# Kernel optimization log

Hardware: AMD Instinct MI355X
Metric: run time of the kernel (lower is better)

## Reference

```python
import jax, jax.numpy as jnp
import numpy as np

G, NPG = 2048, 512          # glimpses, points per glimpse
N0 = G * NPG                # 1,048,576 input points
CPG, CPG2 = 128, 32         # clusters per glimpse at level1/level2
M1, M2 = G * CPG, G * CPG2  # 262144, 65536


def _seg_mean_np(x, ids, m):
    cnt = np.bincount(ids, minlength=m).astype(np.float32)
    out = np.stack([np.bincount(ids, weights=x[:, d], minlength=m) for d in range(x.shape[1])], axis=1)
    return (out / np.maximum(cnt, 1.0)[:, None]).astype(np.float32)


def setup_inputs() -> dict:
    key = jax.random.key(0)
    ks = jax.random.split(key, 16)
    rng = np.random.default_rng(0)
    pos_np = (rng.random((N0, 3)) * 4.0).astype(np.float32)
    # voxel_mean_pool level 0: each point -> a cluster within its glimpse
    g_of_pt = np.arange(N0) // NPG
    out_index0 = (g_of_pt * CPG + rng.integers(0, CPG, N0)).astype(np.int64)
    pos1_np = _seg_mean_np(pos_np, out_index0, M1)
    g_of_c1 = np.arange(M1) // CPG
    out_index1 = (g_of_c1 * CPG2 + rng.integers(0, CPG2, M1)).astype(np.int64)
    pos2_np = _seg_mean_np(pos1_np, out_index1, M2)
    out_index2 = (np.arange(M2) // CPG2).astype(np.int64)  # glimpse id per level-2 point

    def w(k, shp, s=0.05):
        return jax.random.normal(k, shp, dtype=jnp.float32) * s

    return {
        "rgb": jax.random.normal(ks[0], (N0, 1), dtype=jnp.float32),
        "pos": jnp.asarray(pos_np), "pos1": jnp.asarray(pos1_np), "pos2": jnp.asarray(pos2_np),
        "out_index0": jnp.asarray(out_index0), "out_index1": jnp.asarray(out_index1),
        "out_index2": jnp.asarray(out_index2),
        "eps": jax.random.normal(ks[1], (G, 128), dtype=jnp.float32),
        # conv1: local (c_in=1 + 3 -> 16), global (16 -> 32)
        "W1l": w(ks[2], (4, 16)), "b1l": jnp.zeros(16), "W1g": w(ks[3], (16, 32)), "b1g": jnp.zeros(32),
        # conv2: (32+3 -> 64), (64 -> 128)
        "W2l": w(ks[4], (35, 64)), "b2l": jnp.zeros(64), "W2g": w(ks[5], (64, 128)), "b2g": jnp.zeros(128),
        # conv3: (128+3 -> 128), (128 -> 256)
        "W3l": w(ks[6], (131, 128)), "b3l": jnp.zeros(128), "W3g": w(ks[7], (128, 256)), "b3g": jnp.zeros(256),
        "Wlin": w(ks[8], (256, 256)), "blin": jnp.zeros(256),
    }


def _point_conv(x_in, pos_in, pos_out, out_index, Wl, bl, Wg, bg):
    # gather relative position of each input point w.r.t. its output center
    rel = pos_in - pos_out[out_index]                      # [E,3]
    h = jax.nn.celu(jnp.concatenate([x_in, rel], -1) @ Wl + bl)  # per-edge MLP
    m = pos_out.shape[0]
    cnt = jax.ops.segment_sum(jnp.ones((h.shape[0],), h.dtype), out_index, num_segments=m)
    agg = jax.ops.segment_sum(h, out_index, num_segments=m) / jnp.maximum(cnt, 1.0)[:, None]
    return agg @ Wg + bg


def reference(rgb, pos, pos1, pos2, out_index0, out_index1, out_index2, eps,
              W1l, b1l, W1g, b1g, W2l, b2l, W2g, b2g, W3l, b3l, W3g, b3g, Wlin, blin):
    f = rgb  # ar=False path: feature = rgb
    f = jax.nn.celu(_point_conv(f, pos, pos1, out_index0, W1l, b1l, W1g, b1g))   # [M1,32]
    f = jax.nn.celu(_point_conv(f, pos1, pos2, out_index1, W2l, b2l, W2g, b2g))  # [M2,128]
    centers = jnp.zeros((G, 3), f.dtype)  # pos_sample = zeros_like(glimpse__center)
    f = jax.nn.celu(_point_conv(f, pos2, centers, out_index2, W3l, b3l, W3g, b3g))  # [G,256]
    out = f @ Wlin + blin
    mu, sg = jnp.split(out, 2, axis=1)
    sigma = jax.nn.softplus(sg)  # to_sigma
    z = mu + sigma * eps         # Normal.rsample
    z_what, z_mask = jnp.split(z, 2, axis=1)
    return z_what, z_mask, mu, sigma, f
```

## Files before the change

### kernel.cpp

```cpp
#include <hip/hip_runtime.h>
#include <hip/hip_bf16.h>
#include <cstddef>

#define G_   2048
#define NPG_ 512
#define CPG_ 128
#define CPG2_ 32

#define OFF_ZW 0
#define OFF_ZM (G_*64)
#define OFF_MU (2*G_*64)
#define OFF_SG (2*G_*64 + G_*128)
#define OFF_F  (2*G_*64 + 2*G_*128)

typedef __attribute__((ext_vector_type(8))) short bf16x8;
typedef __attribute__((ext_vector_type(4))) float f32x4;
typedef _Float16 f16x2 __attribute__((ext_vector_type(2)));

__device__ __forceinline__ float celu_f(float x)     { return x > 0.f ? x : __expf(x) - 1.f; }
__device__ __forceinline__ float softplus_f(float x) { return fmaxf(x, 0.f) + __logf(1.f + __expf(-fabsf(x))); }
__device__ __forceinline__ unsigned short f2bf(float x) {
    unsigned u = __float_as_uint(x);
    u += 0x7FFFu + ((u >> 16) & 1u);
    return (unsigned short)(u >> 16);
}
__device__ __forceinline__ unsigned pack2(float a, float b) {
    unsigned ua = __float_as_uint(a); ua += 0x7FFFu + ((ua >> 16) & 1u);
    unsigned ub = __float_as_uint(b); ub += 0x7FFFu + ((ub >> 16) & 1u);
    return (ua >> 16) | (ub & 0xFFFF0000u);
}
__device__ __forceinline__ bf16x8 ldb8(const unsigned short* p) {
    union { uint2 u[2]; bf16x8 v; } x;
    x.u[0] = *(const uint2*)p;
    x.u[1] = *(const uint2*)(p + 4);
    return x.v;
}

__global__ void k_prep(const float* __restrict__ W2l, const float* __restrict__ W2g,
                       const float* __restrict__ W3l, const float* __restrict__ W3g,
                       const float* __restrict__ Wlin, const float* __restrict__ W1g,
                       unsigned short* __restrict__ w2lT, unsigned short* __restrict__ w2gT,
                       unsigned short* __restrict__ w3lT, unsigned short* __restrict__ w3gT,
                       unsigned short* __restrict__ wlinT, unsigned short* __restrict__ w1gT)
{
    const int tid = blockIdx.x*256 + threadIdx.x, stride = gridDim.x*256;
    for (int i = tid; i < 64*64; i += stride) {
        const int ch = i >> 6, k = i & 63;
        w2lT[i] = f2bf(k < 35 ? W2l[k*64 + ch] : 0.f);
    }
    for (int i = tid; i < 128*64; i += stride) {
        const int ch = i >> 6, k = i & 63;
        w2gT[i] = f2bf(W2g[k*128 + ch]);
    }
    for (int i = tid; i < 128*160; i += stride) {
        const int ch = i / 160, k = i % 160;
        w3lT[i] = f2bf(k < 131 ? W3l[k*128 + ch] : 0.f);
    }
    for (int i = tid; i < 256*128; i += stride) {
        const int ch = i >> 7, k = i & 127;
        w3gT[i] = f2bf(W3g[k*256 + ch]);
    }
    for (int i = tid; i < 256*256; i += stride) {
        const int ch = i >> 8, k = i & 255;
        wlinT[i] = f2bf(Wlin[k*256 + ch]);
    }
    for (int i = tid; i < 32*40; i += stride) {
        const int ch = i / 40, k = i % 40;
        w1gT[i] = f2bf(k < 16 ? W1g[k*32 + ch] : 0.f);
    }
}

__global__ __launch_bounds__(256, 6) void k_fused(
    const float* __restrict__ rgb, const float* __restrict__ pos, const float* __restrict__ pos1,
    const float* __restrict__ pos2, const int* __restrict__ idx0, const int* __restrict__ idx1,
    const float* __restrict__ W1l, const float* __restrict__ b1l,
    const unsigned short* __restrict__ w1gT, const float* __restrict__ b1g,
    const unsigned short* __restrict__ w2lT, const float* __restrict__ b2l,
    const unsigned short* __restrict__ w2gT, const float* __restrict__ b2g,
    const unsigned short* __restrict__ w3lT, const float* __restrict__ b3l,
    unsigned short* __restrict__ aggws)
{
    const int g = blockIdx.x, t = threadIdx.x;
    const int lane = t & 63, wv = t >> 6;
    const int lr = lane & 15, quad = lane >> 4;

    __shared__ __align__(16) unsigned char smem[27008];
    uint4* const hp4 = (uint4*)smem;
    unsigned short* const aggT  = (unsigned short*)(smem + 16384);
    unsigned short* const xs16  = (unsigned short*)smem;
    unsigned short* const HT    = (unsigned short*)smem;
    unsigned short* const xs3   = (unsigned short*)smem;
    int* const cnt  = (int*)(smem + 25600);
    int* const ctr  = (int*)(smem + 26112);
    int* const cnti = (int*)(smem + 26624);
    int* const wtot = (int*)(smem + 26752);
    unsigned short* const sT   = (unsigned short*)(smem + 18432);
    unsigned short* const agg2 = (unsigned short*)(smem + 18432);
    float* const red  = (float*)(smem + 18432);
    float* const invc = (float*)(smem + 26880);

    if (t < CPG_)  cnt[t]  = 0;
    if (t < CPG2_) cnti[t] = 0;
    int slc_r = 0;
    float relx = 0.f, rely = 0.f, relz = 0.f;
    if (t < CPG_) {
        const int c2 = idx1[g*CPG_ + t];
        slc_r = c2 - g*CPG2_;
        relx = pos1[(g*CPG_ + t)*3 + 0] - pos2[c2*3 + 0];
        rely = pos1[(g*CPG_ + t)*3 + 1] - pos2[c2*3 + 1];
        relz = pos1[(g*CPG_ + t)*3 + 2] - pos2[c2*3 + 2];
    }
    for (int i = t; i < 128*8; i += 256) {
        const int r = i >> 3, j = i & 7;
        ((unsigned*)aggT)[r*18 + 8 + j] = 0u;
    }
    __syncthreads();

    float px0[2], prx[2], pry[2], prz[2];
    int plc[2];
    #pragma unroll
    for (int r = 0; r < 2; r++) {
        const int lp = r*256 + t;
        const int p  = g*NPG_ + lp;
        const int c  = idx0[p];
        plc[r] = c - g*CPG_;
        px0[r] = rgb[p];
        prx[r] = pos[p*3+0] - pos1[c*3+0];
        pry[r] = pos[p*3+1] - pos1[c*3+1];
        prz[r] = pos[p*3+2] - pos1[c*3+2];
        atomicAdd(&cnt[plc[r]], 1);
    }
    if (t < CPG_) atomicAdd(&cnti[slc_r], 1);
    __syncthreads();

    if (t < CPG_) {
        int val = cnt[t];
        const int ln = t & 63;
        #pragma unroll
        for (int d = 1; d < 64; d <<= 1) {
            const int v = __shfl_up(val, d, 64);
            if (ln >= d) val += v;
        }
        ctr[t] = val - cnt[t];
        if (t == 63) *wtot = val;
    }
    if (t < CPG2_) invc[t] = 1.f / fmaxf((float)cnti[t], 1.f);
    __syncthreads();

    const int wtotv = *wtot;

    #pragma unroll
    for (int r = 0; r < 2; r++) {
        unsigned hpk[8];
        #pragma unroll
        for (int j = 0; j < 16; j += 2) {
            const float h0 = celu_f(b1l[j]   + px0[r]*W1l[j]   + prx[r]*W1l[16+j]
                                              + pry[r]*W1l[32+j]   + prz[r]*W1l[48+j]);
            const float h1 = celu_f(b1l[j+1] + px0[r]*W1l[j+1] + prx[r]*W1l[16+j+1]
                                              + pry[r]*W1l[32+j+1] + prz[r]*W1l[48+j+1]);
            union { f16x2 h; unsigned u; } pk;
            pk.h[0] = (_Float16)h0;
            pk.h[1] = (_Float16)h1;
            hpk[j >> 1] = pk.u;
        }
        const int slot = atomicAdd(&ctr[plc[r]], 1) + (plc[r] >= 64 ? wtotv : 0);
        uint4 q0, q1;
        q0.x = hpk[0]; q0.y = hpk[1]; q0.z = hpk[2]; q0.w = hpk[3];
        q1.x = hpk[4]; q1.y = hpk[5]; q1.z = hpk[6]; q1.w = hpk[7];
        hp4[slot]       = q0;
        hp4[512 + slot] = q1;
    }
    __syncthreads();

    const bf16x8 w1g_b0 = *(const bf16x8*)&w1gT[lr*40 + quad*8];
    const bf16x8 w1g_b1 = *(const bf16x8*)&w1gT[(16 + lr)*40 + quad*8];
    const float  b1g_0 = b1g[lr], b1g_1 = b1g[16 + lr];

    {
        const int c = t >> 1, half = t & 1;
        const int n = cnt[c];
        const int base = ctr[c] - n + (c >= 64 ? wtotv : 0);
        const int n0 = (n + 1) >> 1;
        const int sI = base + (half ? n0 : 0);
        const int eI = base + (half ? n  : n0);
        f16x2 acc[8];
        #pragma unroll
        for (int j = 0; j < 8; j++) { union { unsigned u; f16x2 h; } z; z.u = 0u; acc[j] = z.h; }
        for (int i = sI; i < eI; i++) {
            const uint4 a = hp4[i];
            const uint4 b = hp4[512 + i];
            union { unsigned u; f16x2 h; } w;
            w.u = a.x; acc[0] += w.h;  w.u = a.y; acc[1] += w.h;
            w.u = a.z; acc[2] += w.h;  w.u = a.w; acc[3] += w.h;
            w.u = b.x; acc[4] += w.h;  w.u = b.y; acc[5] += w.h;
            w.u = b.z; acc[6] += w.h;  w.u = b.w; acc[7] += w.h;
        }
        #pragma unroll
        for (int j = 0; j < 8; j++) {
            union { unsigned u; f16x2 h; } s, o;
            s.h = acc[j];
            o.u = __shfl_xor(s.u, 1);
            acc[j] += o.h;
        }
        const float inv = 1.f / fmaxf((float)n, 1.f);
        const int ch0 = half * 8, j0 = half * 4;
        float v[8];
        #pragma unroll
        for (int k = 0; k < 4; k++) {
            v[2*k]   = (float)acc[j0+k][0] * inv;
            v[2*k+1] = (float)acc[j0+k][1] * inv;
        }
        uint2 q0, q1;
        q0.x = pack2(v[0], v[1]); q0.y = pack2(v[2], v[3]);
        q1.x = pack2(v[4], v[5]); q1.y = pack2(v[6], v[7]);
        *(uint2*)&aggT[c*36 + ch0]     = q0;
        *(uint2*)&aggT[c*36 + ch0 + 4] = q1;
    }
    __syncthreads();

    f32x4 c1[2][2];
    {
        c1[0][0] = (f32x4){b1g_0, b1g_0, b1g_0, b1g_0};
        c1[0][1] = c1[0][0];
        c1[1][0] = (f32x4){b1g_1, b1g_1, b1g_1, b1g_1};
        c1[1][1] = c1[1][0];
        #pragma unroll
        for (int mt = 0; mt < 2; mt++) {
            const bf16x8 a = ldb8(&aggT[((2*wv + mt)*16 + lr)*36 + quad*8]);
            c1[0][mt] = __builtin_amdgcn_mfma_f32_16x16x32_bf16(a, w1g_b0, c1[0][mt], 0, 0, 0);
            c1[1][mt] = __builtin_amdgcn_mfma_f32_16x16x32_bf16(a, w1g_b1, c1[1][mt], 0, 0, 0);
        }
    }
    __syncthreads();

    {
        const uint4 z4 = {0u, 0u, 0u, 0u};
        for (int i = t; i < 528; i += 256) ((uint4*)sT)[i] = z4;
        for (int i = t; i < 128*5; i += 256) {
            const int r = i / 5, c = 35 + (i - r*5);
            xs16[r*72 + c] = 0;
        }
        for (int i = t; i < 128*3; i += 256) {
            const int r = i / 3, c4 = i - r*3;
            *(uint4*)&xs16[r*72 + 40 + c4*8] = z4;
        }
    }
    #pragma unroll
    for (int nt = 0; nt < 2; nt++)
    #pragma unroll
    for (int mt = 0; mt < 2; mt++)
    #pragma unroll
    for (int r = 0; r < 4; r++) {
        const int cl = (2*wv + mt)*16 + quad*4 + r;
        xs16[cl*72 + nt*16 + lr] = f2bf(celu_f(c1[nt][mt][r]));
    }
    if (t < CPG_) {
        xs16[t*72 + 32] = f2bf(relx);
        xs16[t*72 + 33] = f2bf(rely);
        xs16[t*72 + 34] = f2bf(relz);
    }
    __syncthreads();

    if (t < CPG_) sT[slc_r*132 + t] = 0x3F80;
    float hv[8][4];
    {
        const int chn = wv*16 + lr;
        const bf16x8 bw0 = *(const bf16x8*)&w2lT[chn*64 + quad*8];
        const bf16x8 bw1 = *(const bf16x8*)&w2lT[chn*64 + 32 + quad*8];
        const float bias = b2l[chn];
        #pragma unroll
        for (int m = 0; m < 8; m++) {
            f32x4 acc = (f32x4){bias, bias, bias, bias};
            const bf16x8 a0 = *(const bf16x8*)&xs16[(m*16 + lr)*72 + quad*8];
            const bf16x8 a1 = *(const bf16x8*)&xs16[(m*16 + lr)*72 + 32 + quad*8];
            acc = __builtin_amdgcn_mfma_f32_16x16x32_bf16(a0, bw0, acc, 0, 0, 0);
            acc = __builtin_amdgcn_mfma_f32_16x16x32_bf16(a1, bw1, acc, 0, 0, 0);
            #pragma unroll
            for (int r = 0; r < 4; r++) hv[m][r] = celu_f(acc[r]);
        }
    }
    __syncthreads();

    {
        const int chn = wv*16 + lr;
        #pragma unroll
        for (int m = 0; m < 8; m++) {
            uint2 p;
            p.x = pack2(hv[m][0], hv[m][1]);
            p.y = pack2(hv[m][2], hv[m][3]);
            *(uint2*)&HT[chn*136 + m*16 + quad*4] = p;
        }
    }
    __syncthreads();

    float aggv[2][4];
    {
        const int ch = wv*16 + lr;
        f32x4 acc[2];
        acc[0] = (f32x4){0.f, 0.f, 0.f, 0.f};
        acc[1] = (f32x4){0.f, 0.f, 0.f, 0.f};
        #pragma unroll
        for (int ks = 0; ks < 4; ks++) {
            const bf16x8 b = *(const bf16x8*)&HT[ch*136 + ks*32 + quad*8];
            #pragma unroll
            for (int mt = 0; mt < 2; mt++) {
                const bf16x8 a = ldb8(&sT[(mt*16 + lr)*132 + ks*32 + quad*8]);
                acc[mt] = __builtin_amdgcn_mfma_f32_16x16x32_bf16(a, b, acc[mt], 0, 0, 0);
            }
        }
        #pragma unroll
        for (int mt = 0; mt < 2; mt++)
        #pragma unroll
        for (int r = 0; r < 4; r++)
            aggv[mt][r] = acc[mt][r] * invc[mt*16 + quad*4 + r];
    }
    __syncthreads();

    {
        const int ch = wv*16 + lr;
        #pragma unroll
        for (int mt = 0; mt < 2; mt++)
        #pragma unroll
        for (int r = 0; r < 4; r++)
            agg2[(mt*16 + quad*4 + r)*72 + ch] = f2bf(aggv[mt][r]);
    }
    if (t < CPG2_) {
        #pragma unroll
        for (int d = 0; d < 3; d++)
            xs3[t*168 + 128 + d] = f2bf(pos2[(g*CPG2_ + t)*3 + d]);
    }
    {
        const uint4 z4 = {0u, 0u, 0u, 0u};
        for (int i = t; i < 32*5; i += 256) {
            const int r = i / 5, c = 131 + (i - r*5);
            xs3[r*168 + c] = 0;
        }
        for (int i = t; i < 32*3; i += 256) {
            const int r = i / 3, c4 = i - r*3;
            *(uint4*)&xs3[r*168 + 136 + c4*8] = z4;
        }
    }
    __syncthreads();

    {
        f32x4 acc2[2][2];
        int   chn2[2];
        bf16x8 bw[2][2];
        #pragma unroll
        for (int nt = 0; nt < 2; nt++) {
            chn2[nt] = (wv + nt*4)*16 + lr;
            const float bias = b2g[chn2[nt]];
            #pragma unroll
            for (int mt = 0; mt < 2; mt++) acc2[nt][mt] = (f32x4){bias, bias, bias, bias};
            bw[nt][0] = *(const bf16x8*)&w2gT[chn2[nt]*64 + quad*8];
            bw[nt][1] = *(const bf16x8*)&w2gT[chn2[nt]*64 + 32 + quad*8];
        }
        #pragma unroll
        for (int ks = 0; ks < 2; ks++) {
            #pragma unroll
            for (int mt = 0; mt < 2; mt++) {
                const bf16x8 a = *(const bf16x8*)&agg2[(mt*16 + lr)*72 + ks*32 + quad*8];
                acc2[0][mt] = __builtin_amdgcn_mfma_f32_16x16x32_bf16(a, bw[0][ks], acc2[0][mt], 0, 0, 0);
                acc2[1][mt] = __builtin_amdgcn_mfma_f32_16x16x32_bf16(a, bw[1][ks], acc2[1][mt], 0, 0, 0);
            }
        }
        #pragma unroll
        for (int nt = 0; nt < 2; nt++)
        #pragma unroll
        for (int mt = 0; mt < 2; mt++)
        #pragma unroll
        for (int r = 0; r < 4; r++) {
            const int row = mt*16 + quad*4 + r;
            xs3[row*168 + chn2[nt]] = f2bf(celu_f(acc2[nt][mt][r]));
        }
    }
    __syncthreads();

    {
        f32x4 acc[2][2];
        int chn[2];
        #pragma unroll
        for (int nt = 0; nt < 2; nt++) {
            chn[nt] = (wv + nt*4)*16 + lr;
            const float bias = b3l[chn[nt]];
            #pragma unroll
            for (int mt = 0; mt < 2; mt++) acc[nt][mt] = (f32x4){bias, bias, bias, bias};
        }
        #pragma unroll
        for (int ks = 0; ks < 5; ks++) {
            const bf16x8 b0 = *(const bf16x8*)&w3lT[chn[0]*160 + ks*32 + quad*8];
            const bf16x8 b1 = *(const bf16x8*)&w3lT[chn[1]*160 + ks*32 + quad*8];
            #pragma unroll
            for (int mt = 0; mt < 2; mt++) {
                const bf16x8 a = *(const bf16x8*)&xs3[(mt*16 + lr)*168 + ks*32 + quad*8];
                acc[0][mt] = __builtin_amdgcn_mfma_f32_16x16x32_bf16(a, b0, acc[0][mt], 0, 0, 0);
                acc[1][mt] = __builtin_amdgcn_mfma_f32_16x16x32_bf16(a, b1, acc[1][mt], 0, 0, 0);
            }
        }
        #pragma unroll
        for (int nt = 0; nt < 2; nt++)
        #pragma unroll
        for (int mt = 0; mt < 2; mt++) {
            const float p = celu_f(acc[nt][mt][0]) + celu_f(acc[nt][mt][1])
                          + celu_f(acc[nt][mt][2]) + celu_f(acc[nt][mt][3]);
            red[chn[nt]*9 + mt*4 + quad] = p;
        }
    }
    __syncthreads();

    if (t < 128) {
        const float* rp = &red[t*9];
        float a = 0.f;
        #pragma unroll
        for (int p = 0; p < 8; p++) a += rp[p];
        aggws[(size_t)g*128 + t] = f2bf(a * (1.f/32.f));
    }
}

__global__ __launch_bounds__(256) void k_head(
    const unsigned short* __restrict__ aggws,
    const unsigned short* __restrict__ w3gT, const float* __restrict__ b3g,
    const unsigned short* __restrict__ wlinT, const float* __restrict__ blin,
    const float* __restrict__ eps, float* __restrict__ out)
{
    const int g0 = blockIdx.x * 16, t = threadIdx.x;
    const int lane = t & 63, wv = t >> 6;
    const int lr = lane & 15, quad = lane >> 4;
    __shared__ __align__(16) unsigned short aggB[16*136];
    __shared__ __align__(16) unsigned short f3B[16*264];

    {
        const int row = t >> 4, col8 = (t & 15) * 8;
        const uint4 v = ((const uint4*)aggws)[(size_t)g0*16 + t];
        *(uint4*)&aggB[row*136 + col8] = v;
    }
    __syncthreads();

    {
        f32x4 c3[4];
        int ch3[4];
        #pragma unroll
        for (int nt = 0; nt < 4; nt++) {
            ch3[nt] = (wv + nt*4)*16 + lr;
            const float bias = b3g[ch3[nt]];
            c3[nt] = (f32x4){bias, bias, bias, bias};
        }
        #pragma unroll
        for (int ks = 0; ks < 4; ks++) {
            const bf16x8 a = *(const bf16x8*)&aggB[lr*136 + ks*32 + quad*8];
            #pragma unroll
            for (int nt = 0; nt < 4; nt++) {
                const bf16x8 b = *(const bf16x8*)&w3gT[ch3[nt]*128 + ks*32 + quad*8];
                c3[nt] = __builtin_amdgcn_mfma_f32_16x16x32_bf16(a, b, c3[nt], 0, 0, 0);
            }
        }
        #pragma unroll
        for (int nt = 0; nt < 4; nt++)
        #pragma unroll
        for (int r = 0; r < 4; r++) {
            const int row = quad*4 + r;
            const float v = celu_f(c3[nt][r]);
            out[OFF_F + (size_t)(g0 + row)*256 + ch3[nt]] = v;
            f3B[row*264 + ch3[nt]] = f2bf(v);
        }
    }
    __syncthreads();

    {
        f32x4 cl[4];
        int ch4[4];
        #pragma unroll
        for (int nt = 0; nt < 4; nt++) {
            ch4[nt] = (wv + nt*4)*16 + lr;
            const float bias = blin[ch4[nt]];
            cl[nt] = (f32x4){bias, bias, bias, bias};
        }
        #pragma unroll
        for (int ks = 0; ks < 8; ks++) {
            const bf16x8 a = *(const bf16x8*)&f3B[lr*264 + ks*32 + quad*8];
            #pragma unroll
            for (int nt = 0; nt < 4; nt++) {
                const bf16x8 b = *(const bf16x8*)&wlinT[ch4[nt]*256 + ks*32 + quad*8];
                cl[nt] = __builtin_amdgcn_mfma_f32_16x16x32_bf16(a, b, cl[nt], 0, 0, 0);
            }
        }
        #pragma unroll
        for (int nt = 0; nt < 2; nt++)
        #pragma unroll
        for (int r = 0; r < 4; r++) {
            const int row = quad*4 + r;
            const int g = g0 + row;
            const int ch = ch4[nt];
            const float mu    = cl[nt][r];
            const float sigma = softplus_f(cl[nt + 2][r]);
            const float z     = mu + sigma * eps[(size_t)g*128 + ch];
            out[OFF_MU + (size_t)g*128 + ch] = mu;
            out[OFF_SG + (size_t)g*128 + ch] = sigma;
            if (nt == 0) out[OFF_ZW + (size_t)g*64 + ch] = z;
            else         out[OFF_ZM + (size_t)g*64 + (ch - 64)] = z;
        }
    }
}

extern "C" void kernel_launch(void* const* d_in, const int* in_sizes, int n_in,
                              void* d_out, int out_size, void* d_ws, size_t ws_size,
                              hipStream_t stream)
{
    const float* rgb  = (const float*)d_in[0];
    const float* pos  = (const float*)d_in[1];
    const float* pos1 = (const float*)d_in[2];
    const float* pos2 = (const float*)d_in[3];
    const int*   idx0 = (const int*)d_in[4];
    const int*   idx1 = (const int*)d_in[5];
    const float* eps  = (const float*)d_in[7];
    const float* W1l = (const float*)d_in[8],  *b1l = (const float*)d_in[9];
    const float* W1g = (const float*)d_in[10], *b1g = (const float*)d_in[11];
    const float* W2l = (const float*)d_in[12], *b2l = (const float*)d_in[13];
    const float* W2g = (const float*)d_in[14], *b2g = (const float*)d_in[15];
    const float* W3l = (const float*)d_in[16], *b3l = (const float*)d_in[17];
    const float* W3g = (const float*)d_in[18], *b3g = (const float*)d_in[19];
    const float* Wlin = (const float*)d_in[20], *blin = (const float*)d_in[21];

    unsigned short* w2lT  = (unsigned short*)d_ws;
    unsigned short* w2gT  = w2lT + 64*64;
    unsigned short* w3lT  = w2gT + 128*64;
    unsigned short* w3gT  = w3lT + 128*160;
    unsigned short* wlinT = w3gT + 256*128;
    unsigned short* w1gT  = wlinT + 256*256;
    unsigned short* aggws = w1gT + 32*40;
    float* outp = (float*)d_out;

    k_prep <<<64,    256, 0, stream>>>(W2l, W2g, W3l, W3g, Wlin, W1g,
                                       w2lT, w2gT, w3lT, w3gT, wlinT, w1gT);
    k_fused<<<G_,    256, 0, stream>>>(rgb, pos, pos1, pos2, idx0, idx1,
                                       W1l, b1l, w1gT, b1g,
                                       w2lT, b2l, w2gT, b2g, w3lT, b3l, aggws);
    k_head <<<G_/16, 256, 0, stream>>>(aggws, w3gT, b3g, wlinT, blin, eps, outp);
}
```

Baseline: 156.7 us.

## Shrink LDS row padding, zero-fill MFMA operands in registers, widen head kernel

Reduces the LDS row strides for the level-1 aggregate, conv2 input and conv3 input tiles. Padding columns that used to be zeroed in shared memory are now supplied as zero registers for lanes whose K slice lies past the real data, which drops several zero-fill loops and cuts the shared footprint so more blocks can fit per CU. The final per-channel reduction replaces the shared scratch buffer and its barrier with wave shuffles. The head kernel moves to 512 threads so each wave computes half as many output tiles. The narrower strides may bring LDS bank conflicts, and the head change redistributes work without reducing it.

```diff
diff --git a/kernel.cpp b/kernel.cpp
--- a/kernel.cpp
+++ b/kernel.cpp
@@ -83,21 +83,21 @@
     const int g = blockIdx.x, t = threadIdx.x;
     const int lane = t & 63, wv = t >> 6;
     const int lr = lane & 15, quad = lane >> 4;
-
-    __shared__ __align__(16) unsigned char smem[27008];
+    const bf16x8 z8 = {0,0,0,0,0,0,0,0};
+
+    __shared__ __align__(16) unsigned char smem[25984];
     uint4* const hp4 = (uint4*)smem;
-    unsigned short* const aggT  = (unsigned short*)(smem + 16384);
-    unsigned short* const xs16  = (unsigned short*)smem;
-    unsigned short* const HT    = (unsigned short*)smem;
-    unsigned short* const xs3   = (unsigned short*)smem;
-    int* const cnt  = (int*)(smem + 25600);
-    int* const ctr  = (int*)(smem + 26112);
-    int* const cnti = (int*)(smem + 26624);
-    int* const wtot = (int*)(smem + 26752);
-    unsigned short* const sT   = (unsigned short*)(smem + 18432);
-    unsigned short* const agg2 = (unsigned short*)(smem + 18432);
-    float* const red  = (float*)(smem + 18432);
-    float* const invc = (float*)(smem + 26880);
+    unsigned short* const aggT = (unsigned short*)(smem + 16384);
+    int* const cnt  = (int*)(smem + 21504);
+    int* const ctr  = (int*)(smem + 22016);
+    int* const cnti = (int*)(smem + 22528);
+    int* const wtot = (int*)(smem + 22656);
+    unsigned short* const xs16 = (unsigned short*)smem;
+    unsigned short* const HT   = (unsigned short*)smem;
+    unsigned short* const xs3  = (unsigned short*)smem;
+    unsigned short* const sT   = (unsigned short*)(smem + 17408);
+    unsigned short* const agg2 = (unsigned short*)(smem + 17408);
+    float* const invc = (float*)(smem + 25856);
 
     if (t < CPG_)  cnt[t]  = 0;
     if (t < CPG2_) cnti[t] = 0;
@@ -110,19 +110,14 @@
         rely = pos1[(g*CPG_ + t)*3 + 1] - pos2[c2*3 + 1];
         relz = pos1[(g*CPG_ + t)*3 + 2] - pos2[c2*3 + 2];
     }
-    for (int i = t; i < 128*8; i += 256) {
-        const int r = i >> 3, j = i & 7;
-        ((unsigned*)aggT)[r*18 + 8 + j] = 0u;
-    }
     __syncthreads();
 
     float px0[2], prx[2], pry[2], prz[2];
     int plc[2];
     #pragma unroll
     for (int r = 0; r < 2; r++) {
-        const int lp = r*256 + t;
-        const int p  = g*NPG_ + lp;
-        const int c  = idx0[p];
+        const int p = g*NPG_ + r*256 + t;
+        const int c = idx0[p];
         plc[r] = c - g*CPG_;
         px0[r] = rgb[p];
         prx[r] = pos[p*3+0] - pos1[c*3+0];
@@ -213,8 +208,8 @@
         uint2 q0, q1;
         q0.x = pack2(v[0], v[1]); q0.y = pack2(v[2], v[3]);
         q1.x = pack2(v[4], v[5]); q1.y = pack2(v[6], v[7]);
-        *(uint2*)&aggT[c*36 + ch0]     = q0;
-        *(uint2*)&aggT[c*36 + ch0 + 4] = q1;
+        *(uint2*)&aggT[c*20 + ch0]     = q0;
+        *(uint2*)&aggT[c*20 + ch0 + 4] = q1;
     }
     __syncthreads();
 
@@ -226,7 +221,8 @@
         c1[1][1] = c1[1][0];
         #pragma unroll
         for (int mt = 0; mt < 2; mt++) {
-            const bf16x8 a = ldb8(&aggT[((2*wv + mt)*16 + lr)*36 + quad*8]);
+            bf16x8 a = z8;
+            if (quad < 2) a = ldb8(&aggT[((2*wv + mt)*16 + lr)*20 + quad*8]);
             c1[0][mt] = __builtin_amdgcn_mfma_f32_16x16x32_bf16(a, w1g_b0, c1[0][mt], 0, 0, 0);
             c1[1][mt] = __builtin_amdgcn_mfma_f32_16x16x32_bf16(a, w1g_b1, c1[1][mt], 0, 0, 0);
         }
@@ -238,11 +234,7 @@
         for (int i = t; i < 528; i += 256) ((uint4*)sT)[i] = z4;
         for (int i = t; i < 128*5; i += 256) {
             const int r = i / 5, c = 35 + (i - r*5);
-            xs16[r*72 + c] = 0;
-        }
-        for (int i = t; i < 128*3; i += 256) {
-            const int r = i / 3, c4 = i - r*3;
-            *(uint4*)&xs16[r*72 + 40 + c4*8] = z4;
+            xs16[r*40 + c] = 0;
         }
     }
     #pragma unroll
@@ -252,12 +244,12 @@
     #pragma unroll
     for (int r = 0; r < 4; r++) {
         const int cl = (2*wv + mt)*16 + quad*4 + r;
-        xs16[cl*72 + nt*16 + lr] = f2bf(celu_f(c1[nt][mt][r]));
+        xs16[cl*40 + nt*16 + lr] = f2bf(celu_f(c1[nt][mt][r]));
     }
     if (t < CPG_) {
-        xs16[t*72 + 32] = f2bf(relx);
-        xs16[t*72 + 33] = f2bf(rely);
-        xs16[t*72 + 34] = f2bf(relz);
+        xs16[t*40 + 32] = f2bf(relx);
+        xs16[t*40 + 33] = f2bf(rely);
+        xs16[t*40 + 34] = f2bf(relz);
     }
     __syncthreads();
 
@@ -271,8 +263,9 @@
         #pragma unroll
         for (int m = 0; m < 8; m++) {
             f32x4 acc = (f32x4){bias, bias, bias, bias};
-            const bf16x8 a0 = *(const bf16x8*)&xs16[(m*16 + lr)*72 + quad*8];
-            const bf16x8 a1 = *(const bf16x8*)&xs16[(m*16 + lr)*72 + 32 + quad*8];
+            const bf16x8 a0 = *(const bf16x8*)&xs16[(m*16 + lr)*40 + quad*8];
+            bf16x8 a1 = z8;
+            if (quad == 0) a1 = *(const bf16x8*)&xs16[(m*16 + lr)*40 + 32];
             acc = __builtin_amdgcn_mfma_f32_16x16x32_bf16(a0, bw0, acc, 0, 0, 0);
             acc = __builtin_amdgcn_mfma_f32_16x16x32_bf16(a1, bw1, acc, 0, 0, 0);
             #pragma unroll
@@ -327,24 +320,17 @@
     if (t < CPG2_) {
         #pragma unroll
         for (int d = 0; d < 3; d++)
-            xs3[t*168 + 128 + d] = f2bf(pos2[(g*CPG2_ + t)*3 + d]);
-    }
-    {
-        const uint4 z4 = {0u, 0u, 0u, 0u};
-        for (int i = t; i < 32*5; i += 256) {
-            const int r = i / 5, c = 131 + (i - r*5);
-            xs3[r*168 + c] = 0;
-        }
-        for (int i = t; i < 32*3; i += 256) {
-            const int r = i / 3, c4 = i - r*3;
-            *(uint4*)&xs3[r*168 + 136 + c4*8] = z4;
-        }
-    }
-    __syncthreads();
-
+            xs3[t*136 + 128 + d] = f2bf(pos2[(g*CPG2_ + t)*3 + d]);
+    }
+    if (t < 160) {
+        const int r = t / 5, c = 131 + (t - r*5);
+        xs3[r*136 + c] = 0;
+    }
+    __syncthreads();
+
+    int chn2[2];
     {
         f32x4 acc2[2][2];
-        int   chn2[2];
         bf16x8 bw[2][2];
         #pragma unroll
         for (int nt = 0; nt < 2; nt++) {
@@ -371,53 +357,55 @@
         #pragma unroll
         for (int r = 0; r < 4; r++) {
             const int row = mt*16 + quad*4 + r;
-            xs3[row*168 + chn2[nt]] = f2bf(celu_f(acc2[nt][mt][r]));
+            xs3[row*136 + chn2[nt]] = f2bf(celu_f(acc2[nt][mt][r]));
         }
     }
     __syncthreads();
 
     {
         f32x4 acc[2][2];
-        int chn[2];
-        #pragma unroll
-        for (int nt = 0; nt < 2; nt++) {
-            chn[nt] = (wv + nt*4)*16 + lr;
-            const float bias = b3l[chn[nt]];
-            #pragma unroll
-            for (int mt = 0; mt < 2; mt++) acc[nt][mt] = (f32x4){bias, bias, bias, bias};
-        }
-        #pragma unroll
-        for (int ks = 0; ks < 5; ks++) {
-            const bf16x8 b0 = *(const bf16x8*)&w3lT[chn[0]*160 + ks*32 + quad*8];
-            const bf16x8 b1 = *(const bf16x8*)&w3lT[chn[1]*160 + ks*32 + quad*8];
+        const float b3lv[2] = {b3l[chn2[0]], b3l[chn2[1]]};
+        #pragma unroll
+        for (int nt = 0; nt < 2; nt++)
+        #pragma unroll
+        for (int mt = 0; mt < 2; mt++) acc[nt][mt] = (f32x4){b3lv[nt], b3lv[nt], b3lv[nt], b3lv[nt]};
+        #pragma unroll
+        for (int ks = 0; ks < 4; ks++) {
+            const bf16x8 b0 = *(const bf16x8*)&w3lT[chn2[0]*160 + ks*32 + quad*8];
+            const bf16x8 b1 = *(const bf16x8*)&w3lT[chn2[1]*160 + ks*32 + quad*8];
             #pragma unroll
             for (int mt = 0; mt < 2; mt++) {
-                const bf16x8 a = *(const bf16x8*)&xs3[(mt*16 + lr)*168 + ks*32 + quad*8];
+                const bf16x8 a = *(const bf16x8*)&xs3[(mt*16 + lr)*136 + ks*32 + quad*8];
                 acc[0][mt] = __builtin_amdgcn_mfma_f32_16x16x32_bf16(a, b0, acc[0][mt], 0, 0, 0);
                 acc[1][mt] = __builtin_amdgcn_mfma_f32_16x16x32_bf16(a, b1, acc[1][mt], 0, 0, 0);
             }
         }
-        #pragma unroll
-        for (int nt = 0; nt < 2; nt++)
-        #pragma unroll
-        for (int mt = 0; mt < 2; mt++) {
-            const float p = celu_f(acc[nt][mt][0]) + celu_f(acc[nt][mt][1])
-                          + celu_f(acc[nt][mt][2]) + celu_f(acc[nt][mt][3]);
-            red[chn[nt]*9 + mt*4 + quad] = p;
-        }
-    }
-    __syncthreads();
-
-    if (t < 128) {
-        const float* rp = &red[t*9];
-        float a = 0.f;
-        #pragma unroll
-        for (int p = 0; p < 8; p++) a += rp[p];
-        aggws[(size_t)g*128 + t] = f2bf(a * (1.f/32.f));
-    }
-}
-
-__global__ __launch_bounds__(256) void k_head(
+        {
+            const bf16x8 b0 = *(const bf16x8*)&w3lT[chn2[0]*160 + 128 + quad*8];
+            const bf16x8 b1 = *(const bf16x8*)&w3lT[chn2[1]*160 + 128 + quad*8];
+            #pragma unroll
+            for (int mt = 0; mt < 2; mt++) {
+                bf16x8 a = z8;
+                if (quad == 0) a = *(const bf16x8*)&xs3[(mt*16 + lr)*136 + 128];
+                acc[0][mt] = __builtin_amdgcn_mfma_f32_16x16x32_bf16(a, b0, acc[0][mt], 0, 0, 0);
+                acc[1][mt] = __builtin_amdgcn_mfma_f32_16x16x32_bf16(a, b1, acc[1][mt], 0, 0, 0);
+            }
+        }
+        #pragma unroll
+        for (int nt = 0; nt < 2; nt++) {
+            float s = 0.f;
+            #pragma unroll
+            for (int mt = 0; mt < 2; mt++)
+                s += celu_f(acc[nt][mt][0]) + celu_f(acc[nt][mt][1])
+                   + celu_f(acc[nt][mt][2]) + celu_f(acc[nt][mt][3]);
+            s += __shfl_xor(s, 16);
+            s += __shfl_xor(s, 32);
+            if (quad == 0) aggws[(size_t)g*128 + chn2[nt]] = f2bf(s * (1.f/32.f));
+        }
+    }
+}
+
+__global__ __launch_bounds__(512) void k_head(
     const unsigned short* __restrict__ aggws,
     const unsigned short* __restrict__ w3gT, const float* __restrict__ b3g,
     const unsigned short* __restrict__ wlinT, const float* __restrict__ blin,
@@ -429,7 +417,7 @@
     __shared__ __align__(16) unsigned short aggB[16*136];
     __shared__ __align__(16) unsigned short f3B[16*264];
 
-    {
+    if (t < 256) {
         const int row = t >> 4, col8 = (t & 15) * 8;
         const uint4 v = ((const uint4*)aggws)[(size_t)g0*16 + t];
         *(uint4*)&aggB[row*136 + col8] = v;
@@ -437,11 +425,11 @@
     __syncthreads();
 
     {
-        f32x4 c3[4];
-        int ch3[4];
-        #pragma unroll
-        for (int nt = 0; nt < 4; nt++) {
-            ch3[nt] = (wv + nt*4)*16 + lr;
+        f32x4 c3[2];
+        int ch3[2];
+        #pragma unroll
+        for (int nt = 0; nt < 2; nt++) {
+            ch3[nt] = (wv + nt*8)*16 + lr;
             const float bias = b3g[ch3[nt]];
             c3[nt] = (f32x4){bias, bias, bias, bias};
         }
@@ -449,13 +437,13 @@
         for (int ks = 0; ks < 4; ks++) {
             const bf16x8 a = *(const bf16x8*)&aggB[lr*136 + ks*32 + quad*8];
             #pragma unroll
-            for (int nt = 0; nt < 4; nt++) {
+            for (int nt = 0; nt < 2; nt++) {
                 const bf16x8 b = *(const bf16x8*)&w3gT[ch3[nt]*128 + ks*32 + quad*8];
                 c3[nt] = __builtin_amdgcn_mfma_f32_16x16x32_bf16(a, b, c3[nt], 0, 0, 0);
             }
         }
         #pragma unroll
-        for (int nt = 0; nt < 4; nt++)
+        for (int nt = 0; nt < 2; nt++)
         #pragma unroll
         for (int r = 0; r < 4; r++) {
             const int row = quad*4 + r;
@@ -467,11 +455,11 @@
     __syncthreads();
 
     {
-        f32x4 cl[4];
-        int ch4[4];
-        #pragma unroll
-        for (int nt = 0; nt < 4; nt++) {
-            ch4[nt] = (wv + nt*4)*16 + lr;
+        f32x4 cl[2];
+        int ch4[2];
+        #pragma unroll
+        for (int nt = 0; nt < 2; nt++) {
+            ch4[nt] = (wv + nt*8)*16 + lr;
             const float bias = blin[ch4[nt]];
             cl[nt] = (f32x4){bias, bias, bias, bias};
         }
@@ -479,24 +467,22 @@
         for (int ks = 0; ks < 8; ks++) {
             const bf16x8 a = *(const bf16x8*)&f3B[lr*264 + ks*32 + quad*8];
             #pragma unroll
-            for (int nt = 0; nt < 4; nt++) {
+            for (int nt = 0; nt < 2; nt++) {
                 const bf16x8 b = *(const bf16x8*)&wlinT[ch4[nt]*256 + ks*32 + quad*8];
                 cl[nt] = __builtin_amdgcn_mfma_f32_16x16x32_bf16(a, b, cl[nt], 0, 0, 0);
             }
         }
         #pragma unroll
-        for (int nt = 0; nt < 2; nt++)
-        #pragma unroll
         for (int r = 0; r < 4; r++) {
             const int row = quad*4 + r;
             const int g = g0 + row;
-            const int ch = ch4[nt];
-            const float mu    = cl[nt][r];
-            const float sigma = softplus_f(cl[nt + 2][r]);
+            const int ch = ch4[0];
+            const float mu    = cl[0][r];
+            const float sigma = softplus_f(cl[1][r]);
             const float z     = mu + sigma * eps[(size_t)g*128 + ch];
             out[OFF_MU + (size_t)g*128 + ch] = mu;
             out[OFF_SG + (size_t)g*128 + ch] = sigma;
-            if (nt == 0) out[OFF_ZW + (size_t)g*64 + ch] = z;
+            if (ch < 64) out[OFF_ZW + (size_t)g*64 + ch] = z;
             else         out[OFF_ZM + (size_t)g*64 + (ch - 64)] = z;
         }
     }
@@ -535,5 +521,5 @@
     k_fused<<<G_,    256, 0, stream>>>(rgb, pos, pos1, pos2, idx0, idx1,
                                        W1l, b1l, w1gT, b1g,
                                        w2lT, b2l, w2gT, b2g, w3lT, b3l, aggws);
-    k_head <<<G_/16, 256, 0, stream>>>(aggws, w3gT, b3g, wlinT, blin, eps, outp);
-}
+    k_head <<<G_/16, 512, 0, stream>>>(aggws, w3gT, b3g, wlinT, blin, eps, outp);
+}
```

Measured after the change: 153.1 us, median of 2. 1.02x faster.
